# Optimization experiments

Hardware: AMD Instinct MI355X
Metric: run time of the kernel (lower is better)

Reference implementation:

```python
import jax, jax.numpy as jnp
import numpy as np

B, N, HID = 2, 2048, 896
HQ, HKV, D = 14, 2, 64
THETA = 1000000.0


def setup_inputs() -> dict:
    key = jax.random.key(0)
    ks = jax.random.split(key, 8)
    s = 0.02
    return {
        'hidden_states': jax.random.normal(ks[0], (B, N, HID), jnp.float32),
        'position_ids': jnp.tile(jnp.arange(N, dtype=jnp.int64)[None, :], (B, 1)),
        # weights stored as (in, out) so y = x @ W + b (== torch Linear with W^T)
        'Wq': jax.random.normal(ks[1], (HID, HQ * D), jnp.float32) * s,
        'bq': jnp.zeros((HQ * D,), jnp.float32),
        'Wk': jax.random.normal(ks[2], (HID, HKV * D), jnp.float32) * s,
        'bk': jnp.zeros((HKV * D,), jnp.float32),
        'Wv': jax.random.normal(ks[3], (HID, HKV * D), jnp.float32) * s,
        'bv': jnp.zeros((HKV * D,), jnp.float32),
        'Wg': jax.random.normal(ks[4], (HID, HQ * D), jnp.float32) * s,
        'Wo': jax.random.normal(ks[5], (HQ * D, HID), jnp.float32) * s,
    }


def _rope_cos_sin(position_ids, d, theta):
    inv_freq = 1.0 / (theta ** (jnp.arange(0, d, 2, dtype=jnp.float32) / d))  # [d/2]
    freqs = position_ids.astype(jnp.float32)[..., None] * inv_freq            # [B,N,d/2]
    emb = jnp.concatenate([freqs, freqs], axis=-1)                            # [B,N,d]
    return jnp.cos(emb)[:, None], jnp.sin(emb)[:, None]                       # [B,1,N,d]


def _rotate_half(x):
    h = x.shape[-1] // 2
    return jnp.concatenate([-x[..., h:], x[..., :h]], axis=-1)


def reference(hidden_states, position_ids, Wq, bq, Wk, bk, Wv, bv, Wg, Wo):
    b, n, _ = hidden_states.shape
    g = HQ // HKV  # GQA group size
    Q = (hidden_states @ Wq + bq).reshape(b, n, HQ, D).transpose(0, 2, 1, 3)   # [B,Hq,N,d]
    K = (hidden_states @ Wk + bk).reshape(b, n, HKV, D).transpose(0, 2, 1, 3)  # [B,Hkv,N,d]
    V = (hidden_states @ Wv + bv).reshape(b, n, HKV, D).transpose(0, 2, 1, 3)
    cos, sin = _rope_cos_sin(position_ids, D, THETA)
    Q = Q * cos + _rotate_half(Q) * sin
    K = K * cos + _rotate_half(K) * sin
    scale = 1.0 / np.sqrt(D).astype(np.float32)
    Qg = Q.reshape(b, HKV, g, n, D)
    S = jnp.einsum('bkgnd,bkmd->bkgnm', Qg, K) * scale                         # [B,Hkv,g,N,Nk]
    causal_mask = jnp.arange(n)[:, None] < jnp.arange(n)[None, :]              # q_pos < k_pos
    S = jnp.where(causal_mask, -jnp.inf, S)
    P = jax.nn.softmax(S, axis=-1)
    O = jnp.einsum('bkgnm,bkmd->bkgnd', P, V).reshape(b, HQ, n, D)             # [B,Hq,N,d]
    gate = jax.nn.sigmoid(hidden_states @ Wg).reshape(b, n, HQ, D).transpose(0, 2, 1, 3)
    O = (O * gate).transpose(0, 2, 1, 3).reshape(b, n, HQ * D)
    return O @ Wo
```

## Files before the change

kernel.cpp:

```cpp
#include <hip/hip_runtime.h>
#include <hip/hip_bf16.h>

typedef short s16x4 __attribute__((ext_vector_type(4)));
typedef short s16x8 __attribute__((ext_vector_type(8)));
typedef float f32x4 __attribute__((ext_vector_type(4)));
typedef float f32x16 __attribute__((ext_vector_type(16)));

#define NB 2
#define NSEQ 2048
#define NHID 896
#define NHQ 14
#define NHKV 2
#define HD 64
#define NROW (NB*NSEQ)
#define NCAT 2048
#define PS 40
#define QSC 0.18033688011112042f

__device__ __forceinline__ float bf2f(unsigned short s){
  union { float f; unsigned u; } v; v.u = ((unsigned)s) << 16; return v.f;
}
__device__ __forceinline__ short f2bf(float f){
  union { float f; unsigned u; } v; v.f = f;
  unsigned u = v.u + 0x7fffu + ((v.u >> 16) & 1u);
  return (short)(u >> 16);
}


__global__ void pack_x_kernel(const float* __restrict__ x, short* __restrict__ xb, int n){
  int i = blockIdx.x*256 + threadIdx.x;
  if(i < n) xb[i] = f2bf(x[i]);
}

__global__ __launch_bounds__(256)
void pack_wcat_t_kernel(const float* __restrict__ Wq, const float* __restrict__ Wk,
                        const float* __restrict__ Wv, const float* __restrict__ Wg,
                        short* __restrict__ WcatT){
  __shared__ short T[64][73];
  int c0 = blockIdx.x*64, k0 = blockIdx.y*64;
  const float* src; int width, cb;
  if(c0 < 896){ src = Wq; width = 896; cb = c0; }
  else if(c0 < 1024){ src = Wk; width = 128; cb = c0-896; }
  else if(c0 < 1152){ src = Wv; width = 128; cb = c0-1024; }
  else { src = Wg; width = 896; cb = c0-1152; }
  int tid = threadIdx.x;
  #pragma unroll
  for(int it=0; it<4; ++it){
    int idx = it*256 + tid;
    int r = idx >> 4, q = idx & 15;
    f32x4 v = *(const f32x4*)(src + (long)(k0+r)*width + cb + q*4);
    #pragma unroll
    for(int e=0;e<4;e++) T[r][q*4+e] = f2bf(v[e]);
  }
  __syncthreads();
  #pragma unroll
  for(int it=0; it<2; ++it){
    int idx = it*256 + tid;
    int c = idx >> 3, ch = idx & 7;
    s16x8 o;
    #pragma unroll
    for(int e=0;e<8;e++) o[e] = T[ch*8+e][c];
    *(s16x8*)(WcatT + (long)(c0+c)*NHID + k0 + ch*8) = o;
  }
}

__global__ __launch_bounds__(256)
void pack_wo_t_kernel(const float* __restrict__ Wo, short* __restrict__ WoT){
  __shared__ short T[64][73];
  int c0 = blockIdx.x*64, k0 = blockIdx.y*64;
  int tid = threadIdx.x;
  #pragma unroll
  for(int it=0; it<4; ++it){
    int idx = it*256 + tid;
    int r = idx >> 4, q = idx & 15;
    f32x4 v = *(const f32x4*)(Wo + (long)(k0+r)*896 + c0 + q*4);
    #pragma unroll
    for(int e=0;e<4;e++) T[r][q*4+e] = f2bf(v[e]);
  }
  __syncthreads();
  #pragma unroll
  for(int it=0; it<2; ++it){
    int idx = it*256 + tid;
    int c = idx >> 3, ch = idx & 7;
    s16x8 o;
    #pragma unroll
    for(int e=0;e<8;e++) o[e] = T[ch*8+e][c];
    *(s16x8*)(WoT + (long)(c0+c)*896 + k0 + ch*8) = o;
  }
}

__global__ void rope_table_kernel(const int* __restrict__ pos, float* __restrict__ ct,
                                  float* __restrict__ st){
  int t = blockIdx.x*256 + threadIdx.x;
  if(t >= NROW*32) return;
  int i = t & 31, rn = t >> 5;
  float p = (float)pos[rn];
  float inv = powf(1.0e6f, -(float)i * (1.0f/32.0f));
  float a = p * inv;
  ct[t] = cosf(a);
  st[t] = sinf(a);
}


__global__ __launch_bounds__(256)
void pack_kv_kernel(const short* __restrict__ Kb, const short* __restrict__ Vb,
                    short* __restrict__ Kp, short* __restrict__ Vp){
  __shared__ short Kl[64][72];
  __shared__ short Vl[64][72];
  int j  = blockIdx.x;
  int bh = blockIdx.y;
  int tid = threadIdx.x;
  #pragma unroll
  for(int it=0; it<2; ++it){
    int idx = it*256 + tid;
    int r = idx >> 3, c0 = (idx & 7)*8;
    *(s16x8*)&Kl[r][c0] = *(const s16x8*)(Kb + ((long)bh*NSEQ + j*64 + r)*HD + c0);
    *(s16x8*)&Vl[r][c0] = *(const s16x8*)(Vb + ((long)bh*NSEQ + j*64 + r)*HD + c0);
  }
  __syncthreads();
  long base = ((long)bh*32 + j)*4096;
  #pragma unroll
  for(int it=0; it<2; ++it){
    int c = it*256 + tid;
    int f = c >> 6, l = c & 63;
    int kt = f >> 2, ks = f & 3, h = l >> 5, r5 = l & 31;
    *(s16x8*)(Kp + base + f*512 + l*8) = *(const s16x8*)&Kl[kt*32 + r5][16*ks + 8*h];
    s16x8 o;
    #pragma unroll
    for(int e=0;e<4;e++){
      o[e]   = Vl[16*ks + 4*h + e    ][kt*32 + r5];
      o[4+e] = Vl[16*ks + 4*h + 8 + e][kt*32 + r5];
    }
    *(s16x8*)(Vp + base + f*512 + l*8) = o;
  }
}


template<int EPI>
__global__ __launch_bounds__(256)
void gemm_kernel(const short* __restrict__ A, const short* __restrict__ Bt,
                 int Ncols, int K,
                 const float* __restrict__ bq, const float* __restrict__ bk,
                 const float* __restrict__ bv,
                 const float* __restrict__ ct, const float* __restrict__ st,
                 short* __restrict__ Qb, short* __restrict__ Kb, short* __restrict__ Vb,
                 short* __restrict__ gateb, float* __restrict__ outp)
{
  __shared__ short As[2][128*PS];
  __shared__ short Bs[2][128*PS];

  int tid = threadIdx.x;
  int w = tid >> 6, l = tid & 63;
  int wm = w >> 1, wn = w & 1;

  int bid = blockIdx.y * gridDim.x + blockIdx.x;
  int cpx = (gridDim.x * gridDim.y) >> 3;
  int swz = (bid & 7)*cpx + (bid >> 3);
  int bx = swz % gridDim.x, by = swz / gridDim.x;

  int row0 = by*128;
  int col0 = bx*128;
  int lo = l & 15, hi = l >> 4;

  const short* A0 = A  + (long)row0*K;
  const short* B0 = Bt + (long)col0*K;

  f32x4 acc[4][4];
  #pragma unroll
  for(int mi=0;mi<4;mi++)
    #pragma unroll
    for(int ni=0;ni<4;ni++) acc[mi][ni] = (f32x4){0.f,0.f,0.f,0.f};

  int srow = tid >> 2;
  int scol = (tid & 3)*8;

  s16x8 ra[2], rb[2];
  auto gload = [&](int k0){
    #pragma unroll
    for(int i=0;i<2;i++){
      int row = i*64 + srow;
      ra[i] = *(const s16x8*)(A0 + (long)row*K + k0 + scol);
      rb[i] = *(const s16x8*)(B0 + (long)row*K + k0 + scol);
    }
  };
  auto swrite = [&](int buf){
    #pragma unroll
    for(int i=0;i<2;i++){
      int row = i*64 + srow;
      *(s16x8*)&As[buf][row*PS + scol] = ra[i];
      *(s16x8*)&Bs[buf][row*PS + scol] = rb[i];
    }
  };

  gload(0);
  swrite(0);

  int NIT = K >> 5;
  int cur = 0;
  for(int it=0; it<NIT; ++it){
    __syncthreads();
    if(it+1 < NIT) gload((it+1)*32);

    s16x8 af[4], bf[4];
    #pragma unroll
    for(int mi=0;mi<4;mi++) af[mi] = *(const s16x8*)&As[cur][(wm*64 + 16*mi + lo)*PS + 8*hi];
    #pragma unroll
    for(int ni=0;ni<4;ni++) bf[ni] = *(const s16x8*)&Bs[cur][(wn*64 + 16*ni + lo)*PS + 8*hi];
    #pragma unroll
    for(int mi=0;mi<4;mi++)
      #pragma unroll
      for(int ni=0;ni<4;ni++)
        acc[mi][ni] = __builtin_amdgcn_mfma_f32_16x16x32_bf16(af[mi], bf[ni], acc[mi][ni], 0,0,0);

    if(it+1 < NIT) swrite(cur^1);
    cur ^= 1;
  }

  if(EPI == 1){
    #pragma unroll
    for(int mi=0;mi<4;mi++)
      #pragma unroll
      for(int ni=0;ni<4;ni++)
        #pragma unroll
        for(int rg=0;rg<4;rg++){
          int r = row0 + wm*64 + 16*mi + 4*hi + rg;
          int c = col0 + wn*64 + lo + 16*ni;
          outp[(long)r*Ncols + c] = acc[mi][ni][rg];
        }
  } else {
    int wcol0 = col0 + wn*64;
    int region = (wcol0 < 896) ? 0 : (wcol0 < 1024) ? 1 : (wcol0 < 1152) ? 2 : 3;
    #pragma unroll
    for(int mi=0;mi<4;mi++){
      #pragma unroll
      for(int rg=0;rg<4;rg++){
        int r = row0 + wm*64 + 16*mi + 4*hi + rg;
        int b = r >> 11, n = r & 2047;
        if(region <= 1){
          #pragma unroll
          for(int ni=0;ni<2;ni++){
            int c  = wcol0 + lo + 16*ni;
            int cb = (region==0) ? c : (c-896);
            int hh = cb >> 6, dlo = cb & 63;
            float bl = (region==0) ? bq[c]    : bk[cb];
            float bh = (region==0) ? bq[c+32] : bk[cb+32];
            float ylo = acc[mi][ni  ][rg] + bl;
            float yhi = acc[mi][ni+2][rg] + bh;
            float cs = ct[r*32 + dlo];
            float sn = st[r*32 + dlo];
            float olo = ylo*cs - yhi*sn;
            float ohi = yhi*cs + ylo*sn;
            if(region==0){
              long base = ((long)(b*NHQ + hh)*NSEQ + n)*HD;
              Qb[base + dlo]      = f2bf(olo*QSC);
              Qb[base + dlo + 32] = f2bf(ohi*QSC);
            } else {
              long base = ((long)(b*NHKV + hh)*NSEQ + n)*HD;
              Kb[base + dlo]      = f2bf(olo);
              Kb[base + dlo + 32] = f2bf(ohi);
            }
          }
        } else if(region == 2){
          #pragma unroll
          for(int ni=0;ni<4;ni++){
            int c = wcol0 + lo + 16*ni;
            int cv = c - 1024;
            int hh = cv >> 6, d = cv & 63;
            float y = acc[mi][ni][rg] + bv[cv];
            Vb[((long)(b*NHKV + hh)*NSEQ + n)*HD + d] = f2bf(y);
          }
        } else {
          #pragma unroll
          for(int ni=0;ni<4;ni++){
            int c = wcol0 + lo + 16*ni;
            int cg = c - 1152;
            float y = acc[mi][ni][rg];
            gateb[(long)r*NHID + cg] = f2bf(1.0f/(1.0f + __expf(-y)));
          }
        }
      }
    }
  }
}


__global__ __launch_bounds__(448)
void attn3_kernel(const short* __restrict__ Qb, const short* __restrict__ Kp,
                  const short* __restrict__ Vp, const short* __restrict__ gateb,
                  short* __restrict__ Og, float* __restrict__ Pbuf)
{
  int tid = threadIdx.x;
  int l = tid & 63;
  int q5 = l & 31, h = l >> 5;
  int hg = tid >> 6;

  int s = 119 - blockIdx.x;
  int kvb = blockIdx.y;
  int b = kvb >> 1, kv = kvb & 1;
  int hq = kv*7 + hg;
  int head = kvb*7 + hg;

  int t, ci, nc;
  if(s < 24){ t = s; ci = 0; nc = 1; }
  else if(s < 72){ int r = s-24; t = 24 + (r>>1); ci = r & 1; nc = 2; }
  else { int r = s-72; t = 48 + r/3; ci = r - (r/3)*3; nc = 3; }

  int qg = t*32 + q5;
  int jcausal = (t*32 + 31) >> 6;
  int ng = jcausal + 1;
  int j0, j1;
  if(nc == 1){ j0 = 0; j1 = jcausal; }
  else if(nc == 2){
    int half = (ng + 1) >> 1;
    j0 = ci ? half : 0;
    j1 = ci ? jcausal : (half - 1);
  } else {
    int third = (ng + 2) / 3;
    j0 = ci * third;
    j1 = (ci == 2) ? jcausal : (j0 + third - 1);
  }

  const short* qrow = Qb + ((long)(b*NHQ + hq)*NSEQ + t*32 + q5)*HD;
  s16x8 qf[4];
  #pragma unroll
  for(int ks=0; ks<4; ++ks) qf[ks] = *(const s16x8*)(qrow + 16*ks + 8*h);

  const short* kpb = Kp + (long)kvb*32*4096 + l*8;
  const short* vpb = Vp + (long)kvb*32*4096 + l*8;

  f32x16 oT[2];
  #pragma unroll
  for(int mt=0; mt<2; ++mt)
    #pragma unroll
    for(int rg=0; rg<16; ++rg) oT[mt][rg] = 0.f;
  float m = -__builtin_inff(), lsum = 0.f;

  s16x8 kf[2][4];
  #pragma unroll
  for(int kt=0; kt<2; ++kt)
    #pragma unroll
    for(int ks=0; ks<4; ++ks)
      kf[kt][ks] = *(const s16x8*)(kpb + (long)j0*4096 + (kt*4+ks)*512);

  for(int j=j0; j<=j1; ++j){
    s16x8 vf[2][4];
    #pragma unroll
    for(int mt=0; mt<2; ++mt)
      #pragma unroll
      for(int ss=0; ss<4; ++ss)
        vf[mt][ss] = *(const s16x8*)(vpb + (long)j*4096 + (mt*4+ss)*512);

    f32x16 s2[2];
    #pragma unroll
    for(int kt=0; kt<2; ++kt)
      #pragma unroll
      for(int rg=0; rg<16; ++rg) s2[kt][rg] = 0.f;
    #pragma unroll
    for(int kt=0; kt<2; ++kt)
      #pragma unroll
      for(int ks=0; ks<4; ++ks)
        s2[kt] = __builtin_amdgcn_mfma_f32_32x32x16_bf16(kf[kt][ks], qf[ks], s2[kt], 0,0,0);

    int jn = (j < j1) ? j+1 : j;
    s16x8 kn[2][4];
    #pragma unroll
    for(int kt=0; kt<2; ++kt)
      #pragma unroll
      for(int ks=0; ks<4; ++ks)
        kn[kt][ks] = *(const s16x8*)(kpb + (long)jn*4096 + (kt*4+ks)*512);

    if(j == jcausal){
      #pragma unroll
      for(int kt=0; kt<2; ++kt)
        #pragma unroll
        for(int rg=0; rg<16; ++rg){
          int kl = j*64 + kt*32 + (rg&3) + 8*(rg>>2) + 4*h;
          if(kl > qg) s2[kt][rg] = -__builtin_inff();
        }
    }

    float mA[8];
    #pragma unroll
    for(int w8=0; w8<8; ++w8)
      mA[w8] = fmaxf(fmaxf(s2[0][w8], s2[0][w8+8]), fmaxf(s2[1][w8], s2[1][w8+8]));
    float mx = fmaxf(fmaxf(fmaxf(mA[0],mA[1]), fmaxf(mA[2],mA[3])),
                     fmaxf(fmaxf(mA[4],mA[5]), fmaxf(mA[6],mA[7])));
    mx = fmaxf(mx, __shfl_xor(mx, 32, 64));

    if(__any(mx > m + 8.0f)){
      float mn = fmaxf(m, mx);
      float fac = exp2f(m - mn);
      m = mn;
      lsum *= fac;
      #pragma unroll
      for(int mt=0; mt<2; ++mt)
        #pragma unroll
        for(int rg=0; rg<16; ++rg) oT[mt][rg] *= fac;
    }

    #pragma unroll
    for(int kt=0; kt<2; ++kt)
      #pragma unroll
      for(int rg=0; rg<16; ++rg) s2[kt][rg] = exp2f(s2[kt][rg] - m);
    float sA[8];
    #pragma unroll
    for(int w8=0; w8<8; ++w8)
      sA[w8] = (s2[0][w8] + s2[0][w8+8]) + (s2[1][w8] + s2[1][w8+8]);
    float rs = ((sA[0]+sA[1]) + (sA[2]+sA[3])) + ((sA[4]+sA[5]) + (sA[6]+sA[7]));
    rs += __shfl_xor(rs, 32, 64);
    lsum += rs;

    int pd[2][8];
    #pragma unroll
    for(int kt=0; kt<2; ++kt)
      #pragma unroll
      for(int w8=0; w8<8; ++w8)
        asm("v_cvt_pk_bf16_f32 %0, %1, %2"
            : "=v"(pd[kt][w8]) : "v"(s2[kt][2*w8]), "v"(s2[kt][2*w8+1]));

    #pragma unroll
    for(int ss=0; ss<4; ++ss){
      union { int i4[4]; s16x8 v8; } pf;
      #pragma unroll
      for(int e=0; e<4; ++e) pf.i4[e] = pd[ss>>1][4*(ss&1) + e];
      #pragma unroll
      for(int mt=0; mt<2; ++mt)
        oT[mt] = __builtin_amdgcn_mfma_f32_32x32x16_bf16(vf[mt][ss], pf.v8, oT[mt], 0,0,0);
    }

    #pragma unroll
    for(int kt=0; kt<2; ++kt)
      #pragma unroll
      for(int ks=0; ks<4; ++ks) kf[kt][ks] = kn[kt][ks];
  }

  if(nc == 1){
    float inv = 1.0f/lsum;
    long obase = ((long)(b*NSEQ + t*32 + q5))*NHID + hq*HD;
    #pragma unroll
    for(int mt=0; mt<2; ++mt)
      #pragma unroll
      for(int rq=0; rq<4; ++rq){
        int d0 = mt*32 + 8*rq + 4*h;
        s16x4 g4 = *(const s16x4*)(gateb + obase + d0);
        s16x4 o4;
        #pragma unroll
        for(int e=0; e<4; ++e)
          o4[e] = f2bf(oT[mt][4*rq + e]*inv*bf2f((unsigned short)g4[e]));
        *(s16x4*)(Og + obase + d0) = o4;
      }
  } else {
    int poff = (nc == 2) ? (t-24)*2 : 48 + (t-48)*3;
    float* pb = Pbuf + ((long)head*144 + poff + ci)*2112;
    #pragma unroll
    for(int mt=0; mt<2; ++mt)
      #pragma unroll
      for(int rg=0; rg<16; ++rg){
        int d = mt*32 + (rg&3) + 8*(rg>>2) + 4*h;
        pb[q5*64 + d] = oT[mt][rg];
      }
    if(h == 0){
      pb[2048 + q5] = m;
      pb[2080 + q5] = lsum;
    }
  }
}


__global__ __launch_bounds__(64)
void attn_combine_kernel(const float* __restrict__ Pbuf, const short* __restrict__ gateb,
                         short* __restrict__ Og)
{
  int t = 24 + blockIdx.x;
  int head = blockIdx.y;
  int hg = head % 7; int kvb = head / 7; int b = kvb >> 1; int kv = kvb & 1;
  int hq = kv*7 + hg;
  int nc = (t < 48) ? 2 : 3;
  int poff = (t < 48) ? (t-24)*2 : 48 + (t-48)*3;
  const float* pb0 = Pbuf + ((long)head*144 + poff)*2112;

  int l = threadIdx.x;
  int q5 = l & 31;
  int d0 = (l >> 5)*32;

  float ms[3];
  float M = -__builtin_inff();
  #pragma unroll
  for(int i=0;i<3;i++){
    ms[i] = (i < nc) ? pb0[i*2112 + 2048 + q5] : -__builtin_inff();
    M = fmaxf(M, ms[i]);
  }
  float L = 0.f;
  f32x4 Oa[8];
  #pragma unroll
  for(int c=0;c<8;c++) Oa[c] = (f32x4){0.f,0.f,0.f,0.f};
  #pragma unroll
  for(int i=0;i<3;i++){
    if(i < nc){
      float fac = exp2f(ms[i] - M);
      L += pb0[i*2112 + 2080 + q5] * fac;
      const float* po = pb0 + i*2112 + q5*64 + d0;
      #pragma unroll
      for(int c=0;c<8;c++){
        f32x4 v = *(const f32x4*)(po + 4*c);
        #pragma unroll
        for(int e=0;e<4;e++) Oa[c][e] += v[e]*fac;
      }
    }
  }
  float inv = 1.0f/L;
  long obase = ((long)(b*NSEQ + t*32 + q5))*NHID + hq*HD + d0;
  #pragma unroll
  for(int c=0;c<8;c++){
    s16x4 g4 = *(const s16x4*)(gateb + obase + 4*c);
    s16x4 o4;
    #pragma unroll
    for(int e=0;e<4;e++)
      o4[e] = f2bf(Oa[c][e]*inv*bf2f((unsigned short)g4[e]));
    *(s16x4*)(Og + obase + 4*c) = o4;
  }
}


extern "C" void kernel_launch(void* const* d_in, const int* in_sizes, int n_in,
                              void* d_out, int out_size, void* d_ws, size_t ws_size,
                              hipStream_t stream)
{
  const float* hs  = (const float*)d_in[0];
  const int*   pos = (const int*)d_in[1];
  const float* Wq  = (const float*)d_in[2];
  const float* bq  = (const float*)d_in[3];
  const float* Wk  = (const float*)d_in[4];
  const float* bk  = (const float*)d_in[5];
  const float* Wv  = (const float*)d_in[6];
  const float* bv  = (const float*)d_in[7];
  const float* Wg  = (const float*)d_in[8];
  const float* Wo  = (const float*)d_in[9];
  float* out = (float*)d_out;

  char* p = (char*)d_ws;
  short* Xb    = (short*)p; p += (size_t)NROW*NHID*2;
  short* WcatT = (short*)p; p += (size_t)NCAT*NHID*2;
  short* WoT   = (short*)p; p += (size_t)NHID*NHID*2;
  float* ct    = (float*)p; p += (size_t)NROW*32*4;
  float* st    = (float*)p; p += (size_t)NROW*32*4;
  short* Qb    = (short*)p; p += (size_t)NB*NHQ*NSEQ*HD*2;
  short* Kb    = (short*)p; p += (size_t)NB*NHKV*NSEQ*HD*2;
  short* Vb    = (short*)p; p += (size_t)NB*NHKV*NSEQ*HD*2;
  short* Kp    = (short*)p; p += (size_t)4*32*4096*2;
  short* Vp    = (short*)p; p += (size_t)4*32*4096*2;
  short* gateb = (short*)p; p += (size_t)NROW*NHID*2;
  short* Og    = (short*)p; p += (size_t)NROW*NHID*2;
  float* Pbuf  = (float*)p; p += (size_t)28*144*2112*4;

  pack_x_kernel<<<(NROW*NHID+255)/256, 256, 0, stream>>>(hs, Xb, NROW*NHID);
  pack_wcat_t_kernel<<<dim3(NCAT/64, NHID/64), 256, 0, stream>>>(Wq, Wk, Wv, Wg, WcatT);
  pack_wo_t_kernel<<<dim3(NHID/64, NHID/64), 256, 0, stream>>>(Wo, WoT);
  rope_table_kernel<<<(NROW*32+255)/256, 256, 0, stream>>>(pos, ct, st);

  gemm_kernel<0><<<dim3(NCAT/128, NROW/128), 256, 0, stream>>>(
      Xb, WcatT, NCAT, NHID, bq, bk, bv, ct, st, Qb, Kb, Vb, gateb, nullptr);

  pack_kv_kernel<<<dim3(32, 4), 256, 0, stream>>>(Kb, Vb, Kp, Vp);

  attn3_kernel<<<dim3(120, 4), 448, 0, stream>>>(Qb, Kp, Vp, gateb, Og, Pbuf);
  attn_combine_kernel<<<dim3(40, 28), 64, 0, stream>>>(Pbuf, gateb, Og);

  gemm_kernel<1><<<dim3(NHID/128, NROW/128), 256, 0, stream>>>(
      Og, WoT, NHID, NHID, nullptr, nullptr, nullptr, nullptr, nullptr,
      nullptr, nullptr, nullptr, nullptr, out);
}
```

Before: 125.3 us.

## Process two query heads per wave in attention to reuse K/V fragments

```diff
diff --git a/kernel.cpp b/kernel.cpp
--- a/kernel.cpp
+++ b/kernel.cpp
@@ -284,21 +284,24 @@
 }
 
 
-__global__ __launch_bounds__(448)
-void attn3_kernel(const short* __restrict__ Qb, const short* __restrict__ Kp,
+__global__ __launch_bounds__(256)
+void attn5_kernel(const short* __restrict__ Qb, const short* __restrict__ Kp,
                   const short* __restrict__ Vp, const short* __restrict__ gateb,
                   short* __restrict__ Og, float* __restrict__ Pbuf)
 {
   int tid = threadIdx.x;
   int l = tid & 63;
   int q5 = l & 31, h = l >> 5;
-  int hg = tid >> 6;
+  int w = tid >> 6;
+  bool dual = (w < 3);
+  int hgA = dual ? 2*w : 6;
+  int hgB = 2*w + 1;
 
   int s = 119 - blockIdx.x;
   int kvb = blockIdx.y;
   int b = kvb >> 1, kv = kvb & 1;
-  int hq = kv*7 + hg;
-  int head = kvb*7 + hg;
+  int hqA = kv*7 + hgA, hqB = kv*7 + hgB;
+  int headA = kvb*7 + hgA, headB = kvb*7 + hgB;
 
   int t, ci, nc;
   if(s < 24){ t = s; ci = 0; nc = 1; }
@@ -320,20 +323,27 @@
     j1 = (ci == 2) ? jcausal : (j0 + third - 1);
   }
 
-  const short* qrow = Qb + ((long)(b*NHQ + hq)*NSEQ + t*32 + q5)*HD;
+  const short* qrowA = Qb + ((long)(b*NHQ + hqA)*NSEQ + t*32 + q5)*HD;
   s16x8 qf[4];
   #pragma unroll
-  for(int ks=0; ks<4; ++ks) qf[ks] = *(const s16x8*)(qrow + 16*ks + 8*h);
+  for(int ks=0; ks<4; ++ks) qf[ks] = *(const s16x8*)(qrowA + 16*ks + 8*h);
+  const short* qrowB = Qb + ((long)(b*NHQ + hqB)*NSEQ + t*32 + q5)*HD;
+  s16x8 qfB[4];
+  if(dual){
+    #pragma unroll
+    for(int ks=0; ks<4; ++ks) qfB[ks] = *(const s16x8*)(qrowB + 16*ks + 8*h);
+  }
 
   const short* kpb = Kp + (long)kvb*32*4096 + l*8;
   const short* vpb = Vp + (long)kvb*32*4096 + l*8;
 
-  f32x16 oT[2];
+  f32x16 oT[2], oTB[2];
   #pragma unroll
   for(int mt=0; mt<2; ++mt)
     #pragma unroll
-    for(int rg=0; rg<16; ++rg) oT[mt][rg] = 0.f;
+    for(int rg=0; rg<16; ++rg){ oT[mt][rg] = 0.f; oTB[mt][rg] = 0.f; }
   float m = -__builtin_inff(), lsum = 0.f;
+  float mB = -__builtin_inff(), lsumB = 0.f;
 
   s16x8 kf[2][4];
   #pragma unroll
@@ -428,6 +438,78 @@
         oT[mt] = __builtin_amdgcn_mfma_f32_32x32x16_bf16(vf[mt][ss], pf.v8, oT[mt], 0,0,0);
     }
 
+    if(dual){
+      f32x16 s2B[2];
+      #pragma unroll
+      for(int kt=0; kt<2; ++kt)
+        #pragma unroll
+        for(int rg=0; rg<16; ++rg) s2B[kt][rg] = 0.f;
+      #pragma unroll
+      for(int kt=0; kt<2; ++kt)
+        #pragma unroll
+        for(int ks=0; ks<4; ++ks)
+          s2B[kt] = __builtin_amdgcn_mfma_f32_32x32x16_bf16(kf[kt][ks], qfB[ks], s2B[kt], 0,0,0);
+
+      if(j == jcausal){
+        #pragma unroll
+        for(int kt=0; kt<2; ++kt)
+          #pragma unroll
+          for(int rg=0; rg<16; ++rg){
+            int kl = j*64 + kt*32 + (rg&3) + 8*(rg>>2) + 4*h;
+            if(kl > qg) s2B[kt][rg] = -__builtin_inff();
+          }
+      }
+
+      float mAB[8];
+      #pragma unroll
+      for(int w8=0; w8<8; ++w8)
+        mAB[w8] = fmaxf(fmaxf(s2B[0][w8], s2B[0][w8+8]), fmaxf(s2B[1][w8], s2B[1][w8+8]));
+      float mxB = fmaxf(fmaxf(fmaxf(mAB[0],mAB[1]), fmaxf(mAB[2],mAB[3])),
+                        fmaxf(fmaxf(mAB[4],mAB[5]), fmaxf(mAB[6],mAB[7])));
+      mxB = fmaxf(mxB, __shfl_xor(mxB, 32, 64));
+
+      if(__any(mxB > mB + 8.0f)){
+        float mnB = fmaxf(mB, mxB);
+        float facB = exp2f(mB - mnB);
+        mB = mnB;
+        lsumB *= facB;
+        #pragma unroll
+        for(int mt=0; mt<2; ++mt)
+          #pragma unroll
+          for(int rg=0; rg<16; ++rg) oTB[mt][rg] *= facB;
+      }
+
+      #pragma unroll
+      for(int kt=0; kt<2; ++kt)
+        #pragma unroll
+        for(int rg=0; rg<16; ++rg) s2B[kt][rg] = exp2f(s2B[kt][rg] - mB);
+      float sAB[8];
+      #pragma unroll
+      for(int w8=0; w8<8; ++w8)
+        sAB[w8] = (s2B[0][w8] + s2B[0][w8+8]) + (s2B[1][w8] + s2B[1][w8+8]);
+      float rsB = ((sAB[0]+sAB[1]) + (sAB[2]+sAB[3])) + ((sAB[4]+sAB[5]) + (sAB[6]+sAB[7]));
+      rsB += __shfl_xor(rsB, 32, 64);
+      lsumB += rsB;
+
+      int pdB[2][8];
+      #pragma unroll
+      for(int kt=0; kt<2; ++kt)
+        #pragma unroll
+        for(int w8=0; w8<8; ++w8)
+          asm("v_cvt_pk_bf16_f32 %0, %1, %2"
+              : "=v"(pdB[kt][w8]) : "v"(s2B[kt][2*w8]), "v"(s2B[kt][2*w8+1]));
+
+      #pragma unroll
+      for(int ss=0; ss<4; ++ss){
+        union { int i4[4]; s16x8 v8; } pfB;
+        #pragma unroll
+        for(int e=0; e<4; ++e) pfB.i4[e] = pdB[ss>>1][4*(ss&1) + e];
+        #pragma unroll
+        for(int mt=0; mt<2; ++mt)
+          oTB[mt] = __builtin_amdgcn_mfma_f32_32x32x16_bf16(vf[mt][ss], pfB.v8, oTB[mt], 0,0,0);
+      }
+    }
+
     #pragma unroll
     for(int kt=0; kt<2; ++kt)
       #pragma unroll
@@ -436,7 +518,7 @@
 
   if(nc == 1){
     float inv = 1.0f/lsum;
-    long obase = ((long)(b*NSEQ + t*32 + q5))*NHID + hq*HD;
+    long obase = ((long)(b*NSEQ + t*32 + q5))*NHID + hqA*HD;
     #pragma unroll
     for(int mt=0; mt<2; ++mt)
       #pragma unroll
@@ -449,9 +531,25 @@
           o4[e] = f2bf(oT[mt][4*rq + e]*inv*bf2f((unsigned short)g4[e]));
         *(s16x4*)(Og + obase + d0) = o4;
       }
+    if(dual){
+      float invB = 1.0f/lsumB;
+      long obaseB = ((long)(b*NSEQ + t*32 + q5))*NHID + hqB*HD;
+      #pragma unroll
+      for(int mt=0; mt<2; ++mt)
+        #pragma unroll
+        for(int rq=0; rq<4; ++rq){
+          int d0 = mt*32 + 8*rq + 4*h;
+          s16x4 g4 = *(const s16x4*)(gateb + obaseB + d0);
+          s16x4 o4;
+          #pragma unroll
+          for(int e=0; e<4; ++e)
+            o4[e] = f2bf(oTB[mt][4*rq + e]*invB*bf2f((unsigned short)g4[e]));
+          *(s16x4*)(Og + obaseB + d0) = o4;
+        }
+    }
   } else {
     int poff = (nc == 2) ? (t-24)*2 : 48 + (t-48)*3;
-    float* pb = Pbuf + ((long)head*144 + poff + ci)*2112;
+    float* pb = Pbuf + ((long)headA*144 + poff + ci)*2112;
     #pragma unroll
     for(int mt=0; mt<2; ++mt)
       #pragma unroll
@@ -462,6 +560,20 @@
     if(h == 0){
       pb[2048 + q5] = m;
       pb[2080 + q5] = lsum;
+    }
+    if(dual){
+      float* pbB = Pbuf + ((long)headB*144 + poff + ci)*2112;
+      #pragma unroll
+      for(int mt=0; mt<2; ++mt)
+        #pragma unroll
+        for(int rg=0; rg<16; ++rg){
+          int d = mt*32 + (rg&3) + 8*(rg>>2) + 4*h;
+          pbB[q5*64 + d] = oTB[mt][rg];
+        }
+      if(h == 0){
+        pbB[2048 + q5] = mB;
+        pbB[2080 + q5] = lsumB;
+      }
     }
   }
 }
@@ -563,7 +675,7 @@
 
   pack_kv_kernel<<<dim3(32, 4), 256, 0, stream>>>(Kb, Vb, Kp, Vp);
 
-  attn3_kernel<<<dim3(120, 4), 448, 0, stream>>>(Qb, Kp, Vp, gateb, Og, Pbuf);
+  attn5_kernel<<<dim3(120, 4), 256, 0, stream>>>(Qb, Kp, Vp, gateb, Og, Pbuf);
   attn_combine_kernel<<<dim3(40, 28), 64, 0, stream>>>(Pbuf, gateb, Og);
 
   gemm_kernel<1><<<dim3(NHID/128, NROW/128), 256, 0, stream>>>(
```

Measured after the change: 139.8 us. 1.12x slower.
